# Kernel optimization log

Hardware: AMD Instinct MI355X
Metric: run time of the kernel (lower is better)

The kernel has to match this reference:

```python
import jax, jax.numpy as jnp
import numpy as np

D_MODEL = 1024
N_HEADS = 16
D_HEAD = 64
SEQ = 2048
BATCH = 2
ATTN_SCALE = float(np.sqrt(D_HEAD))  # cfg.use_attn_scale = True
NEG_INF = -1e9


def setup_inputs() -> dict:
    key = jax.random.key(0)
    ks = jax.random.split(key, 8)
    s = 0.02
    return {
        "query_input": jax.random.normal(ks[0], (BATCH, SEQ, D_MODEL), jnp.float32),
        "key_input": jax.random.normal(ks[1], (BATCH, SEQ, D_MODEL), jnp.float32),
        "value_input": jax.random.normal(ks[2], (BATCH, SEQ, D_MODEL), jnp.float32),
        "W_Q": jax.random.normal(ks[3], (N_HEADS, D_MODEL, D_HEAD), jnp.float32) * s,
        "W_K": jax.random.normal(ks[4], (N_HEADS, D_MODEL, D_HEAD), jnp.float32) * s,
        "W_V": jax.random.normal(ks[5], (N_HEADS, D_MODEL, D_HEAD), jnp.float32) * s,
        "W_O": jax.random.normal(ks[6], (N_HEADS, D_HEAD, D_MODEL), jnp.float32) * s,
        "b_Q": jnp.zeros((N_HEADS, D_HEAD), jnp.float32),
        "b_K": jnp.zeros((N_HEADS, D_HEAD), jnp.float32),
        "b_V": jnp.zeros((N_HEADS, D_HEAD), jnp.float32),
        "b_O": jnp.zeros((D_MODEL,), jnp.float32),
    }


def reference(query_input, key_input, value_input, W_Q, W_K, W_V, W_O, b_Q, b_K, b_V, b_O):
    # QKV projections: [batch, pos, d_model] x [head, d_model, d_head] -> [batch, pos, head, d_head]
    q = jnp.einsum("bpd,hde->bphe", query_input, W_Q) + b_Q
    k = jnp.einsum("bpd,hde->bphe", key_input, W_K) + b_K
    v = jnp.einsum("bpd,hde->bphe", value_input, W_V) + b_V

    # attn scores [batch, head, query_pos, key_pos]
    scores = jnp.einsum("bqhe,bkhe->bhqk", q, k) / ATTN_SCALE

    # causal mask (attn_type == 'global'): tril over [n_ctx, n_ctx] sliced to seq
    causal = jnp.tril(jnp.ones((SEQ, SEQ), bool))
    scores = jnp.where(causal[None, None, :, :], scores, NEG_INF)

    pattern = jax.nn.softmax(scores, axis=-1)

    # z: [batch, query_pos, head, d_head]
    z = jnp.einsum("bhqk,bkhe->bqhe", pattern, v)

    # output projection: [batch, pos, d_model]
    out = jnp.einsum("bqhe,hed->bqd", z, W_O) + b_O
    return out
```

## Files before the change

kernel.cpp:

```cpp
#include <hip/hip_runtime.h>
#include <stdint.h>


typedef __attribute__((ext_vector_type(8))) short short8;
typedef __attribute__((ext_vector_type(4))) float floatx4;
typedef __attribute__((ext_vector_type(4))) unsigned int uintx4;

#define MFMA16(a, b, c) __builtin_amdgcn_mfma_f32_16x16x32_bf16(a, b, c, 0, 0, 0)

__device__ __forceinline__ unsigned short f2b(float f) {
  unsigned int u = __builtin_bit_cast(unsigned int, f);
  u = (u + 0x7fffu + ((u >> 16) & 1u)) >> 16;
  return (unsigned short)u;
}
__device__ __forceinline__ float exp2f_fast(float x) {
#if __has_builtin(__builtin_amdgcn_exp2f)
  return __builtin_amdgcn_exp2f(x);
#else
  return exp2f(x);
#endif
}
__device__ __forceinline__ unsigned int pack2_bf16(float lo, float hi) {
#if __has_builtin(__builtin_amdgcn_perm)
  return __builtin_amdgcn_perm(__builtin_bit_cast(unsigned int, hi),
                               __builtin_bit_cast(unsigned int, lo), 0x07060302u);
#else
  return (__builtin_bit_cast(unsigned int, lo) >> 16) |
         (__builtin_bit_cast(unsigned int, hi) & 0xffff0000u);
#endif
}

__device__ __forceinline__ void async_copy16(void* lds, const void* g) {
  __builtin_amdgcn_global_load_lds(
      (const __attribute__((address_space(1))) unsigned int*)g,
      (__attribute__((address_space(3))) unsigned int*)lds, 16, 0, 0);
}

__device__ __forceinline__ void xpose4(floatx4& v, int lane) {
  {
    float s0 = __shfl_xor(v[1], 1, 64);
    float s1 = __shfl_xor(v[0], 1, 64);
    float s2 = __shfl_xor(v[3], 1, 64);
    float s3 = __shfl_xor(v[2], 1, 64);
    if (lane & 1) { v[0] = s0; v[2] = s2; } else { v[1] = s1; v[3] = s3; }
  }
  {
    float s0 = __shfl_xor(v[2], 2, 64);
    float s1 = __shfl_xor(v[3], 2, 64);
    float s2 = __shfl_xor(v[0], 2, 64);
    float s3 = __shfl_xor(v[1], 2, 64);
    if (lane & 2) { v[0] = s0; v[1] = s1; } else { v[2] = s2; v[3] = s3; }
  }
}

__global__ __launch_bounds__(256) void conv_x3(const float* __restrict__ a,
                                               const float* __restrict__ b,
                                               const float* __restrict__ c,
                                               unsigned short* __restrict__ out) {
  const float* in = (blockIdx.y == 0) ? a : ((blockIdx.y == 1) ? b : c);
  size_t i = (size_t)blockIdx.x * 256 + threadIdx.x;
  float4 v = ((const float4*)in)[i];
  ushort4 u;
  u.x = f2b(v.x); u.y = f2b(v.y); u.z = f2b(v.z); u.w = f2b(v.w);
  ((ushort4*)(out + (size_t)blockIdx.y * 4194304))[i] = u;
}

__global__ __launch_bounds__(256) void conv_w3(const float* __restrict__ a,
                                               const float* __restrict__ b,
                                               const float* __restrict__ c,
                                               unsigned short* __restrict__ out) {
  __shared__ float T[64][65];
  const float* in = (blockIdx.y == 0) ? a : ((blockIdx.y == 1) ? b : c);
  const int t = threadIdx.x, rr = t >> 4, cc = t & 15;
  const int h = blockIdx.x >> 4, d0 = (blockIdx.x & 15) << 6;
#pragma unroll
  for (int it = 0; it < 4; ++it) {
    int dl = it * 16 + rr;
    float4 v = *(const float4*)&in[(size_t)h * 65536 + (size_t)(d0 + dl) * 64 + cc * 4];
    T[dl][cc * 4 + 0] = v.x; T[dl][cc * 4 + 1] = v.y;
    T[dl][cc * 4 + 2] = v.z; T[dl][cc * 4 + 3] = v.w;
  }
  __syncthreads();
  unsigned short* ob = out + (size_t)blockIdx.y * 1048576;
#pragma unroll
  for (int it = 0; it < 4; ++it) {
    int e = it * 16 + rr;
    ushort4 u;
    u.x = f2b(T[cc * 4 + 0][e]); u.y = f2b(T[cc * 4 + 1][e]);
    u.z = f2b(T[cc * 4 + 2][e]); u.w = f2b(T[cc * 4 + 3][e]);
    *(ushort4*)&ob[(size_t)(h * 64 + e) * 1024 + d0 + cc * 4] = u;
  }
}

__global__ __launch_bounds__(256) void conv_wo(const float* __restrict__ in,
                                               unsigned short* __restrict__ out) {
  __shared__ float T[64][65];
  const int t = threadIdx.x, rr = t >> 4, cc = t & 15;
  const int r0 = (blockIdx.x & 15) << 6;
  const int c0 = (blockIdx.x >> 4) << 6;
#pragma unroll
  for (int it = 0; it < 4; ++it) {
    int rl = it * 16 + rr;
    float4 v = *(const float4*)&in[(size_t)(r0 + rl) * 1024 + c0 + cc * 4];
    T[rl][cc * 4 + 0] = v.x; T[rl][cc * 4 + 1] = v.y;
    T[rl][cc * 4 + 2] = v.z; T[rl][cc * 4 + 3] = v.w;
  }
  __syncthreads();
#pragma unroll
  for (int it = 0; it < 4; ++it) {
    int dl = it * 16 + rr;
    ushort4 u;
    u.x = f2b(T[cc * 4 + 0][dl]); u.y = f2b(T[cc * 4 + 1][dl]);
    u.z = f2b(T[cc * 4 + 2][dl]); u.w = f2b(T[cc * 4 + 3][dl]);
    *(ushort4*)&out[(size_t)(c0 + dl) * 1024 + r0 + cc * 4] = u;
  }
}

__global__ __launch_bounds__(256) void gemm128(
    const short* __restrict__ A0, const short* __restrict__ A1,
    const short* __restrict__ A2, const short* __restrict__ B0,
    const short* __restrict__ B1, const short* __restrict__ B2,
    const float* __restrict__ bias0, const float* __restrict__ bias1,
    const float* __restrict__ bias2, unsigned short* __restrict__ ob0,
    unsigned short* __restrict__ ob1, unsigned short* __restrict__ ob2,
    float* __restrict__ outf, int qkv, float qscale) {
  __shared__ short As[128 * 32];
  __shared__ short Bs[128 * 32];

  const int z = blockIdx.z;
  const short* A = (z == 0) ? A0 : (z == 1) ? A1 : A2;
  const short* Bt = (z == 0) ? B0 : (z == 1) ? B1 : B2;

  const int tid = threadIdx.x;
  const int lane = tid & 63, w = tid >> 6;
  const int quad = lane >> 4, col = lane & 15;
  const int m0 = blockIdx.y * 128, n0 = blockIdx.x * 128;
  const int wm = (w >> 1) * 64, wn = (w & 1) * 64;

  floatx4 acc[4][4] = {};

  const int lr = lane >> 2, gc = (lane & 3) ^ ((lane >> 3) & 3);
  const short* ga = A + (size_t)(m0 + w * 32 + lr) * 1024 + gc * 8;
  const short* gb = Bt + (size_t)(n0 + w * 32 + lr) * 1024 + gc * 8;
  short* la = &As[(w * 32) * 32];
  short* lb = &Bs[(w * 32) * 32];
  const int asw = (col >> 1) & 3;

  for (int k0 = 0; k0 < 1024; k0 += 32) {
    async_copy16(la, ga);
    async_copy16(la + 16 * 32, ga + 16 * 1024);
    async_copy16(lb, gb);
    async_copy16(lb + 16 * 32, gb + 16 * 1024);
    ga += 32; gb += 32;
    __syncthreads();
    short8 af[4], bf[4];
#pragma unroll
    for (int mi = 0; mi < 4; ++mi)
      af[mi] = *(const short8*)&As[(wm + mi * 16 + col) * 32 + ((quad ^ asw) * 8)];
#pragma unroll
    for (int nj = 0; nj < 4; ++nj)
      bf[nj] = *(const short8*)&Bs[(wn + nj * 16 + col) * 32 + ((quad ^ asw) * 8)];
#pragma unroll
    for (int mi = 0; mi < 4; ++mi)
#pragma unroll
      for (int nj = 0; nj < 4; ++nj)
        acc[mi][nj] = MFMA16(af[mi], bf[nj], acc[mi][nj]);
    __syncthreads();
  }

  const float* bias = (z == 0) ? bias0 : (z == 1) ? bias1 : bias2;
  unsigned short* outb = (z == 0) ? ob0 : (z == 1) ? ob1 : ob2;
  const int mode = qkv ? ((z == 2) ? 2 : 1) : 0;
  const float scale = (qkv && z == 0) ? qscale : 1.0f;

  float bv[4];
#pragma unroll
  for (int nj = 0; nj < 4; ++nj) bv[nj] = bias[n0 + wn + nj * 16 + col];

  if (mode == 2) {
#pragma unroll
    for (int mi = 0; mi < 4; ++mi)
#pragma unroll
      for (int nj = 0; nj < 4; ++nj) {
        int m = m0 + wm + mi * 16 + quad * 4;
        int n = n0 + wn + nj * 16 + col;
        int bb = m >> 11, s = m & 2047, h = n >> 6, e = n & 63;
        ushort4 u;
        u.x = f2b(acc[mi][nj][0] + bv[nj]);
        u.y = f2b(acc[mi][nj][1] + bv[nj]);
        u.z = f2b(acc[mi][nj][2] + bv[nj]);
        u.w = f2b(acc[mi][nj][3] + bv[nj]);
        *(ushort4*)&outb[(((size_t)bb * 16 + h) * 64 + e) * 2048 + s] = u;
      }
  } else {
#pragma unroll
    for (int mi = 0; mi < 4; ++mi)
#pragma unroll
      for (int nj = 0; nj < 4; ++nj) {
        floatx4 v;
#pragma unroll
        for (int r = 0; r < 4; ++r) v[r] = (acc[mi][nj][r] + bv[nj]) * scale;
        xpose4(v, lane);
        int m = m0 + wm + mi * 16 + quad * 4 + (col & 3);
        int nb = n0 + wn + nj * 16 + (col & ~3);
        if (mode == 0) {
          *(floatx4*)&outf[(size_t)m * 1024 + nb] = v;
        } else {
          int bb = m >> 11, s = m & 2047, h = nb >> 6, e = nb & 63;
          ushort4 u;
          u.x = f2b(v[0]); u.y = f2b(v[1]); u.z = f2b(v[2]); u.w = f2b(v[3]);
          *(ushort4*)&outb[(((size_t)bb * 16 + h) * 2048 + s) * 64 + e] = u;
        }
      }
  }
}

__device__ __forceinline__ void exchange4(const unsigned int* u01,
                                          const unsigned int* u23, int srcA,
                                          int srcB, bool hiq, short8& pf0,
                                          short8& pf1) {
  unsigned int xA0 = (unsigned int)__shfl((int)u01[0], srcA, 64);
  unsigned int xA1 = (unsigned int)__shfl((int)u01[1], srcA, 64);
  unsigned int yA0 = (unsigned int)__shfl((int)u23[0], srcA, 64);
  unsigned int yA1 = (unsigned int)__shfl((int)u23[1], srcA, 64);
  unsigned int xB0 = (unsigned int)__shfl((int)u01[0], srcB, 64);
  unsigned int xB1 = (unsigned int)__shfl((int)u01[1], srcB, 64);
  unsigned int yB0 = (unsigned int)__shfl((int)u23[0], srcB, 64);
  unsigned int yB1 = (unsigned int)__shfl((int)u23[1], srcB, 64);
  uintx4 v0;
  v0.x = hiq ? xA1 : xA0; v0.y = hiq ? yA1 : yA0;
  v0.z = hiq ? xB1 : xB0; v0.w = hiq ? yB1 : yB0;
  pf0 = __builtin_bit_cast(short8, v0);
  xA0 = (unsigned int)__shfl((int)u01[2], srcA, 64);
  xA1 = (unsigned int)__shfl((int)u01[3], srcA, 64);
  yA0 = (unsigned int)__shfl((int)u23[2], srcA, 64);
  yA1 = (unsigned int)__shfl((int)u23[3], srcA, 64);
  xB0 = (unsigned int)__shfl((int)u01[2], srcB, 64);
  xB1 = (unsigned int)__shfl((int)u01[3], srcB, 64);
  yB0 = (unsigned int)__shfl((int)u23[2], srcB, 64);
  yB1 = (unsigned int)__shfl((int)u23[3], srcB, 64);
  uintx4 v1;
  v1.x = hiq ? xA1 : xA0; v1.y = hiq ? yA1 : yA0;
  v1.z = hiq ? xB1 : xB0; v1.w = hiq ? yB1 : yB0;
  pf1 = __builtin_bit_cast(short8, v1);
}

__global__ __launch_bounds__(256) void attn(const short* __restrict__ q,
                                            const short* __restrict__ k,
                                            const short* __restrict__ vt,
                                            unsigned short* __restrict__ z) {
  __shared__ short Ks[64 * 64];
  __shared__ short Vs[64 * 64];

  const int tid = threadIdx.x;
  const int lane = tid & 63, w = tid >> 6;
  const int quad = lane >> 4, col = lane & 15;
  const int qt = 31 - (blockIdx.x >> 5), bh = blockIdx.x & 31;
  const int q0 = qt * 64, qw0 = q0 + w * 16;
  const size_t base = (size_t)bh * (2048 * 64);

  const short* qp = q + base + (size_t)(qw0 + col) * 64 + quad * 8;
  short8 bq0 = *(const short8*)qp;
  short8 bq1 = *(const short8*)(qp + 32);

  floatx4 o[4] = {};
  float m_run = -1e30f, l_run = 0.f;

  const short* kg = k + base;
  const short* vg = vt + base;
  const int ksw = col & 7;
  const int slr = lane >> 3, sgc = (lane & 7) ^ slr;
  const int srcA = ((quad & 1) << 5) + col, srcB = srcA + 16;
  const bool hiq = (quad & 2) != 0;

  for (int t = 0; t <= qt; ++t) {
    const int kv0 = t * 64;
    {
      const short* kr = kg + (size_t)(kv0 + w * 16 + slr) * 64 + sgc * 8;
      async_copy16(&Ks[(w * 16) * 64], kr);
      async_copy16(&Ks[(w * 16 + 8) * 64], kr + 8 * 64);
      const short* vr = vg + (size_t)(w * 16 + slr) * 2048 + kv0 + sgc * 8;
      async_copy16(&Vs[(w * 16) * 64], vr);
      async_copy16(&Vs[(w * 16 + 8) * 64], vr + 8 * 2048);
    }
    __syncthreads();

    const bool diag = (t == qt);
    const int mtmax = diag ? w : 3;

    floatx4 st[4];
#pragma unroll
    for (int mt = 0; mt < 4; ++mt) {
      if (mt <= mtmax) {
        const short* kb = &Ks[(mt * 16 + col) * 64];
        short8 ka0 = *(const short8*)(kb + (quad ^ ksw) * 8);
        short8 ka1 = *(const short8*)(kb + ((quad + 4) ^ ksw) * 8);
        floatx4 a = {0.f, 0.f, 0.f, 0.f};
        a = MFMA16(ka0, bq0, a);
        a = MFMA16(ka1, bq1, a);
        if (diag && mt == mtmax) {
#pragma unroll
          for (int r = 0; r < 4; ++r)
            if (quad * 4 + r > col) a[r] = -1e9f;
        }
        st[mt] = a;
      }
    }

    float pmax = -3e38f;
#pragma unroll
    for (int mt = 0; mt < 4; ++mt)
      if (mt <= mtmax) {
#pragma unroll
        for (int r = 0; r < 4; ++r) pmax = fmaxf(pmax, st[mt][r]);
      }
    pmax = fmaxf(pmax, __shfl_xor(pmax, 16, 64));
    pmax = fmaxf(pmax, __shfl_xor(pmax, 32, 64));
    float mnew = fmaxf(m_run, pmax);
    float alpha = exp2f_fast(m_run - mnew);
    m_run = mnew;

    unsigned int u01[4], u23[4];
    float lsum = 0.f;
#pragma unroll
    for (int mt = 0; mt < 4; ++mt) {
      if (mt <= mtmax) {
        float p0 = exp2f_fast(st[mt][0] - mnew);
        float p1 = exp2f_fast(st[mt][1] - mnew);
        float p2 = exp2f_fast(st[mt][2] - mnew);
        float p3 = exp2f_fast(st[mt][3] - mnew);
        lsum += (p0 + p1) + (p2 + p3);
        u01[mt] = pack2_bf16(p0, p1);
        u23[mt] = pack2_bf16(p2, p3);
      } else {
        u01[mt] = 0u; u23[mt] = 0u;
      }
    }
    lsum += __shfl_xor(lsum, 16, 64);
    lsum += __shfl_xor(lsum, 32, 64);
    l_run = l_run * alpha + lsum;

    short8 pf0, pf1;
    exchange4(u01, u23, srcA, srcB, hiq, pf0, pf1);

#pragma unroll
    for (int et = 0; et < 4; ++et) {
      const short* vb = &Vs[(et * 16 + col) * 64];
      short8 va0 = *(const short8*)(vb + (quad ^ ksw) * 8);
      short8 va1 = *(const short8*)(vb + ((quad + 4) ^ ksw) * 8);
      floatx4 t0 = o[et];
#pragma unroll
      for (int r = 0; r < 4; ++r) t0[r] *= alpha;
      t0 = MFMA16(va0, pf0, t0);
      t0 = MFMA16(va1, pf1, t0);
      o[et] = t0;
    }
    __syncthreads();
  }

  const int b = bh >> 4, h = bh & 15;
#if __has_builtin(__builtin_amdgcn_rcpf)
  const float invl = __builtin_amdgcn_rcpf(l_run);
#else
  const float invl = 1.f / l_run;
#endif
  unsigned short* zr = z + (((size_t)b * 2048 + qw0 + col) * 16 + h) * 64;
#pragma unroll
  for (int et = 0; et < 4; ++et) {
    ushort4 u;
    u.x = f2b(o[et][0] * invl); u.y = f2b(o[et][1] * invl);
    u.z = f2b(o[et][2] * invl); u.w = f2b(o[et][3] * invl);
    *(ushort4*)&zr[et * 16 + quad * 4] = u;
  }
}

extern "C" void kernel_launch(void* const* d_in, const int* in_sizes, int n_in,
                              void* d_out, int out_size, void* d_ws, size_t ws_size,
                              hipStream_t stream) {
  (void)in_sizes; (void)n_in; (void)out_size; (void)ws_size;
  const float* Xq = (const float*)d_in[0];
  const float* Xk = (const float*)d_in[1];
  const float* Xv = (const float*)d_in[2];
  const float* WQ = (const float*)d_in[3];
  const float* WK = (const float*)d_in[4];
  const float* WV = (const float*)d_in[5];
  const float* WO = (const float*)d_in[6];
  const float* bQ = (const float*)d_in[7];
  const float* bK = (const float*)d_in[8];
  const float* bV = (const float*)d_in[9];
  const float* bO = (const float*)d_in[10];
  float* out = (float*)d_out;

  unsigned short* xqb = (unsigned short*)d_ws;
  unsigned short* xkb = xqb + 4194304;
  unsigned short* xvb = xkb + 4194304;
  unsigned short* wqt = xvb + 4194304;
  unsigned short* wkt = wqt + 1048576;
  unsigned short* wvt = wkt + 1048576;
  unsigned short* wot = wvt + 1048576;
  unsigned short* qb = wot + 1048576;
  unsigned short* kb = qb + 4194304;
  unsigned short* vtb = kb + 4194304;
  unsigned short* zb = vtb + 4194304;

  conv_x3<<<dim3(4096, 3), 256, 0, stream>>>(Xq, Xk, Xv, xqb);
  conv_w3<<<dim3(256, 3), 256, 0, stream>>>(WQ, WK, WV, wqt);
  conv_wo<<<256, 256, 0, stream>>>(WO, wot);

  const float qscale = 0.125f * 1.44269504088896f;
  gemm128<<<dim3(8, 32, 3), 256, 0, stream>>>(
      (const short*)xqb, (const short*)xkb, (const short*)xvb,
      (const short*)wqt, (const short*)wkt, (const short*)wvt, bQ, bK, bV, qb,
      kb, vtb, nullptr, 1, qscale);

  attn<<<1024, 256, 0, stream>>>((const short*)qb, (const short*)kb,
                                 (const short*)vtb, zb);

  gemm128<<<dim3(8, 32, 1), 256, 0, stream>>>(
      (const short*)zb, (const short*)zb, (const short*)zb, (const short*)wot,
      (const short*)wot, (const short*)wot, bO, bO, bO, nullptr, nullptr,
      nullptr, out, 0, 1.0f);
}
```

Before: 245.2 us.

## Double-buffer LDS in GEMM and attention, use K16 MFMA for PV

Both the projection GEMM and the attention kernel now keep two LDS buffers, so the next K/V or A/B tile is fetched asynchronously while the current one is computed, and one barrier per iteration is dropped. The attention PV product uses the 16x16x16 bf16 MFMA where available, which consumes the softmax probabilities straight from registers, removes the cross-lane shuffle exchange, and skips masked diagonal subtiles. The GEMM grid is flattened to a 1D launch with an x-major block ordering for better reuse of the weight tiles. The cost is doubled shared memory per block, which may lower occupancy, and the single barrier per iteration relies on the async copies having completed when that barrier is reached.

```diff
diff --git a/kernel.cpp b/kernel.cpp
--- a/kernel.cpp
+++ b/kernel.cpp
@@ -3,10 +3,19 @@
 
 
 typedef __attribute__((ext_vector_type(8))) short short8;
+typedef __attribute__((ext_vector_type(4))) short short4v;
 typedef __attribute__((ext_vector_type(4))) float floatx4;
 typedef __attribute__((ext_vector_type(4))) unsigned int uintx4;
+typedef __attribute__((ext_vector_type(2))) unsigned int uint2v;
 
 #define MFMA16(a, b, c) __builtin_amdgcn_mfma_f32_16x16x32_bf16(a, b, c, 0, 0, 0)
+
+#if __has_builtin(__builtin_amdgcn_mfma_f32_16x16x16bf16_1k)
+#define HAVE_K16 1
+#define MFMAK16(a, b, c) __builtin_amdgcn_mfma_f32_16x16x16bf16_1k(a, b, c, 0, 0, 0)
+#else
+#define HAVE_K16 0
+#endif
 
 __device__ __forceinline__ unsigned short f2b(float f) {
   unsigned int u = __builtin_bit_cast(unsigned int, f);
@@ -124,17 +133,24 @@
     const float* __restrict__ bias2, unsigned short* __restrict__ ob0,
     unsigned short* __restrict__ ob1, unsigned short* __restrict__ ob2,
     float* __restrict__ outf, int qkv, float qscale) {
-  __shared__ short As[128 * 32];
-  __shared__ short Bs[128 * 32];
-
-  const int z = blockIdx.z;
+  __shared__ short As[2][128 * 32];
+  __shared__ short Bs[2][128 * 32];
+
+  const int nz = qkv ? 3 : 1;
+  const int ngroups = 32 * nz;
+  const int L = blockIdx.x;
+  const int x = L / ngroups;
+  const int r = L - x * ngroups;
+  const int y = r / nz;
+  const int z = r - y * nz;
+
   const short* A = (z == 0) ? A0 : (z == 1) ? A1 : A2;
   const short* Bt = (z == 0) ? B0 : (z == 1) ? B1 : B2;
 
   const int tid = threadIdx.x;
   const int lane = tid & 63, w = tid >> 6;
   const int quad = lane >> 4, col = lane & 15;
-  const int m0 = blockIdx.y * 128, n0 = blockIdx.x * 128;
+  const int m0 = y * 128, n0 = x * 128;
   const int wm = (w >> 1) * 64, wn = (w & 1) * 64;
 
   floatx4 acc[4][4] = {};
@@ -142,30 +158,38 @@
   const int lr = lane >> 2, gc = (lane & 3) ^ ((lane >> 3) & 3);
   const short* ga = A + (size_t)(m0 + w * 32 + lr) * 1024 + gc * 8;
   const short* gb = Bt + (size_t)(n0 + w * 32 + lr) * 1024 + gc * 8;
-  short* la = &As[(w * 32) * 32];
-  short* lb = &Bs[(w * 32) * 32];
+  const int lofs = (w * 32) * 32;
   const int asw = (col >> 1) & 3;
 
+  async_copy16(&As[0][lofs], ga);
+  async_copy16(&As[0][lofs + 16 * 32], ga + 16 * 1024);
+  async_copy16(&Bs[0][lofs], gb);
+  async_copy16(&Bs[0][lofs + 16 * 32], gb + 16 * 1024);
+
+  int p = 0;
   for (int k0 = 0; k0 < 1024; k0 += 32) {
-    async_copy16(la, ga);
-    async_copy16(la + 16 * 32, ga + 16 * 1024);
-    async_copy16(lb, gb);
-    async_copy16(lb + 16 * 32, gb + 16 * 1024);
-    ga += 32; gb += 32;
     __syncthreads();
+    if (k0 + 32 < 1024) {
+      const short* ga2 = ga + (k0 + 32);
+      const short* gb2 = gb + (k0 + 32);
+      async_copy16(&As[p ^ 1][lofs], ga2);
+      async_copy16(&As[p ^ 1][lofs + 16 * 32], ga2 + 16 * 1024);
+      async_copy16(&Bs[p ^ 1][lofs], gb2);
+      async_copy16(&Bs[p ^ 1][lofs + 16 * 32], gb2 + 16 * 1024);
+    }
     short8 af[4], bf[4];
 #pragma unroll
     for (int mi = 0; mi < 4; ++mi)
-      af[mi] = *(const short8*)&As[(wm + mi * 16 + col) * 32 + ((quad ^ asw) * 8)];
+      af[mi] = *(const short8*)&As[p][(wm + mi * 16 + col) * 32 + ((quad ^ asw) * 8)];
 #pragma unroll
     for (int nj = 0; nj < 4; ++nj)
-      bf[nj] = *(const short8*)&Bs[(wn + nj * 16 + col) * 32 + ((quad ^ asw) * 8)];
+      bf[nj] = *(const short8*)&Bs[p][(wn + nj * 16 + col) * 32 + ((quad ^ asw) * 8)];
 #pragma unroll
     for (int mi = 0; mi < 4; ++mi)
 #pragma unroll
       for (int nj = 0; nj < 4; ++nj)
         acc[mi][nj] = MFMA16(af[mi], bf[nj], acc[mi][nj]);
-    __syncthreads();
+    p ^= 1;
   }
 
   const float* bias = (z == 0) ? bias0 : (z == 1) ? bias1 : bias2;
@@ -199,7 +223,7 @@
       for (int nj = 0; nj < 4; ++nj) {
         floatx4 v;
 #pragma unroll
-        for (int r = 0; r < 4; ++r) v[r] = (acc[mi][nj][r] + bv[nj]) * scale;
+        for (int rr = 0; rr < 4; ++rr) v[rr] = (acc[mi][nj][rr] + bv[nj]) * scale;
         xpose4(v, lane);
         int m = m0 + wm + mi * 16 + quad * 4 + (col & 3);
         int nb = n0 + wn + nj * 16 + (col & ~3);
@@ -215,6 +239,7 @@
   }
 }
 
+#if !HAVE_K16
 __device__ __forceinline__ void exchange4(const unsigned int* u01,
                                           const unsigned int* u23, int srcA,
                                           int srcB, bool hiq, short8& pf0,
@@ -244,13 +269,25 @@
   v1.z = hiq ? xB1 : xB0; v1.w = hiq ? yB1 : yB0;
   pf1 = __builtin_bit_cast(short8, v1);
 }
+#endif
+
+__device__ __forceinline__ void stage_kv(short* Kbuf, short* Vbuf,
+                                         const short* kg, const short* vg,
+                                         int kv0, int w, int slr, int sgc) {
+  const short* kr = kg + (size_t)(kv0 + w * 16 + slr) * 64 + sgc * 8;
+  async_copy16(&Kbuf[(w * 16) * 64], kr);
+  async_copy16(&Kbuf[(w * 16 + 8) * 64], kr + 8 * 64);
+  const short* vr = vg + (size_t)(w * 16 + slr) * 2048 + kv0 + sgc * 8;
+  async_copy16(&Vbuf[(w * 16) * 64], vr);
+  async_copy16(&Vbuf[(w * 16 + 8) * 64], vr + 8 * 2048);
+}
 
 __global__ __launch_bounds__(256) void attn(const short* __restrict__ q,
                                             const short* __restrict__ k,
                                             const short* __restrict__ vt,
                                             unsigned short* __restrict__ z) {
-  __shared__ short Ks[64 * 64];
-  __shared__ short Vs[64 * 64];
+  __shared__ short Ks[2][64 * 64];
+  __shared__ short Vs[2][64 * 64];
 
   const int tid = threadIdx.x;
   const int lane = tid & 63, w = tid >> 6;
@@ -270,21 +307,19 @@
   const short* vg = vt + base;
   const int ksw = col & 7;
   const int slr = lane >> 3, sgc = (lane & 7) ^ slr;
+#if !HAVE_K16
   const int srcA = ((quad & 1) << 5) + col, srcB = srcA + 16;
   const bool hiq = (quad & 2) != 0;
+#endif
+
+  stage_kv(Ks[0], Vs[0], kg, vg, 0, w, slr, sgc);
+  int p = 0;
 
   for (int t = 0; t <= qt; ++t) {
+    __syncthreads();
+    if (t < qt) stage_kv(Ks[p ^ 1], Vs[p ^ 1], kg, vg, (t + 1) * 64, w, slr, sgc);
+
     const int kv0 = t * 64;
-    {
-      const short* kr = kg + (size_t)(kv0 + w * 16 + slr) * 64 + sgc * 8;
-      async_copy16(&Ks[(w * 16) * 64], kr);
-      async_copy16(&Ks[(w * 16 + 8) * 64], kr + 8 * 64);
-      const short* vr = vg + (size_t)(w * 16 + slr) * 2048 + kv0 + sgc * 8;
-      async_copy16(&Vs[(w * 16) * 64], vr);
-      async_copy16(&Vs[(w * 16 + 8) * 64], vr + 8 * 2048);
-    }
-    __syncthreads();
-
     const bool diag = (t == qt);
     const int mtmax = diag ? w : 3;
 
@@ -292,7 +327,7 @@
 #pragma unroll
     for (int mt = 0; mt < 4; ++mt) {
       if (mt <= mtmax) {
-        const short* kb = &Ks[(mt * 16 + col) * 64];
+        const short* kb = &Ks[p][(mt * 16 + col) * 64];
         short8 ka0 = *(const short8*)(kb + (quad ^ ksw) * 8);
         short8 ka1 = *(const short8*)(kb + ((quad + 4) ^ ksw) * 8);
         floatx4 a = {0.f, 0.f, 0.f, 0.f};
@@ -340,12 +375,36 @@
     lsum += __shfl_xor(lsum, 32, 64);
     l_run = l_run * alpha + lsum;
 
+#if HAVE_K16
+    short4v pb[4];
+#pragma unroll
+    for (int mt = 0; mt < 4; ++mt) {
+      uint2v uu;
+      uu.x = u01[mt]; uu.y = u23[mt];
+      pb[mt] = __builtin_bit_cast(short4v, uu);
+    }
+#pragma unroll
+    for (int et = 0; et < 4; ++et) {
+      const short* vrow = &Vs[p][(et * 16 + col) * 64];
+      floatx4 t0 = o[et];
+#pragma unroll
+      for (int r = 0; r < 4; ++r) t0[r] *= alpha;
+#pragma unroll
+      for (int mt = 0; mt < 4; ++mt) {
+        if (mt <= mtmax) {
+          int c = mt * 2 + (quad >> 1);
+          short4v va = *(const short4v*)&vrow[((c ^ ksw) * 8) + (quad & 1) * 4];
+          t0 = MFMAK16(va, pb[mt], t0);
+        }
+      }
+      o[et] = t0;
+    }
+#else
     short8 pf0, pf1;
     exchange4(u01, u23, srcA, srcB, hiq, pf0, pf1);
-
 #pragma unroll
     for (int et = 0; et < 4; ++et) {
-      const short* vb = &Vs[(et * 16 + col) * 64];
+      const short* vb = &Vs[p][(et * 16 + col) * 64];
       short8 va0 = *(const short8*)(vb + (quad ^ ksw) * 8);
       short8 va1 = *(const short8*)(vb + ((quad + 4) ^ ksw) * 8);
       floatx4 t0 = o[et];
@@ -355,7 +414,8 @@
       t0 = MFMA16(va1, pf1, t0);
       o[et] = t0;
     }
-    __syncthreads();
+#endif
+    p ^= 1;
   }
 
   const int b = bh >> 4, h = bh & 15;
@@ -408,7 +468,7 @@
   conv_wo<<<256, 256, 0, stream>>>(WO, wot);
 
   const float qscale = 0.125f * 1.44269504088896f;
-  gemm128<<<dim3(8, 32, 3), 256, 0, stream>>>(
+  gemm128<<<768, 256, 0, stream>>>(
       (const short*)xqb, (const short*)xkb, (const short*)xvb,
       (const short*)wqt, (const short*)wkt, (const short*)wvt, bQ, bK, bV, qb,
       kb, vtb, nullptr, 1, qscale);
@@ -416,7 +476,7 @@
   attn<<<1024, 256, 0, stream>>>((const short*)qb, (const short*)kb,
                                  (const short*)vtb, zb);
 
-  gemm128<<<dim3(8, 32, 1), 256, 0, stream>>>(
+  gemm128<<<256, 256, 0, stream>>>(
       (const short*)zb, (const short*)zb, (const short*)zb, (const short*)wot,
       (const short*)wot, (const short*)wot, bO, bO, bO, nullptr, nullptr,
       nullptr, out, 0, 1.0f);
```

New measurement: 246.7 us. About the same (+0.6%).
